# Kernel tuning notes

Measured on AMD Instinct MI355X. Metric: run time of the kernel, lower is better.

Reference implementation:

```python
import jax, jax.numpy as jnp
import numpy as np
from jax import lax

E, L, S, F = 4, 8, 512, 32
SAMPLE_SIZE = 512
BATCH_LEN = 64
TRAIN_ENVS = [0, 1, 2]


def setup_inputs() -> dict:
    key = jax.random.key(0)
    k1, k2 = jax.random.split(key)
    data_len = jax.random.randint(k2, (E, L), S // 2, S + 1).astype(jnp.int32)
    matrix = jax.random.normal(k1, (E, L, S, F), dtype=jnp.float32)
    # zero-pad samples beyond each (env,label) length, as shape_to_matrix does
    mask = (jnp.arange(S)[None, None, :, None] < data_len[:, :, None, None])
    matrix = matrix * mask.astype(jnp.float32)
    params = jnp.eye(F, dtype=jnp.float32)
    return {"matrix": matrix, "params": params, "data_len": data_len}


def _pair_indices():
    train_idx, test_idx = [], []
    for i in range(E):
        for j in range(E):
            idx = i * E + j
            if i < j:
                test_idx.append(idx)
                if i in TRAIN_ENVS and j in TRAIN_ENVS:
                    train_idx.append(idx)
    return np.array(train_idx), np.array(test_idx)


def reference(matrix, params, data_len):
    # normalize by mean per-(env,label,feature) std (torch.std is unbiased -> ddof=1)
    std = jnp.std(matrix, axis=2, ddof=1).mean()
    m = matrix / std
    bw = 1.06 * (S ** (-1.0 / 5.0)) * jnp.std(m, axis=2, ddof=1).mean()
    lenf = data_len.astype(jnp.float32)                     # [E,L]
    proj = jnp.einsum('elsf,fg->elsg', m, params)           # [E,L,S,F]

    left = lax.stop_gradient(proj.min())
    right = lax.stop_gradient(proj.max())
    delta = (right - left) / SAMPLE_SIZE
    grid = jnp.linspace(left, right, SAMPLE_SIZE)           # [G]
    divisor = jnp.sqrt(2.0 * jnp.pi) * bw

    n_chunks = SAMPLE_SIZE // BATCH_LEN
    grid_chunks = grid.reshape(n_chunks, BATCH_LEN)
    inv2bw2 = 0.5 / (bw * bw)
    pad_count = (float(S) - lenf)[:, :, None, None]         # [E,L,1,1]
    lend = lenf[:, :, None, None]

    def step(carry, pts):
        # Gaussian KDE kernel: offset^(d^2) == exp(-0.5*d^2/bw^2)
        d2 = (proj[..., None] - pts) ** 2                   # [E,L,S,F,C]
        ksum = jnp.exp(-inv2bw2 * d2).sum(axis=2)           # [E,L,F,C]
        corr = pad_count * jnp.exp(-inv2bw2 * pts ** 2)     # zero-padding correction
        red = (ksum - corr) / lend                          # [E,L,F,C]
        diff = jnp.abs(red[:, None] - red[None, :]).sum(-1) # [E,E,L,F]
        return carry + diff, None

    store, _ = lax.scan(step, jnp.zeros((E, E, L, F), dtype=proj.dtype), grid_chunks)
    store_dis = (store / divisor).reshape(E * E, L, F)

    train_idx, test_idx = _pair_indices()
    test_results = (store_dis[test_idx] * delta / 2.0).max(axis=0)    # [L,F]
    train_results = (store_dis[train_idx] * delta / 2.0).max(axis=0)  # [L,F]
    train_dis = train_results.max(axis=0).mean()
    test_dis = test_results.max(axis=0).mean()
    return train_results, test_results, train_dis, test_dis
```

## Files before the change

### kernel.cpp

```cpp
#include <hip/hip_runtime.h>
#include <float.h>


#if __has_builtin(__builtin_amdgcn_exp2f)
__device__ __forceinline__ float fast_exp2(float x) { return __builtin_amdgcn_exp2f(x); }
#else
__device__ __forceinline__ float fast_exp2(float x) { return exp2f(x); }
#endif

#define MAXR 150
#define PADL 160
#define HW   840
#define WOFF 163
#define WFULL 336

#define PT_OFF    0
#define SX_OFF    524288
#define SXX_OFF   532480
#define MIN_OFF   540672
#define MAX_OFF   540928
#define CNT_OFF   541184

__global__ __launch_bounds__(256) void stage_prep(const float* __restrict__ matrix,
                                                  const float* __restrict__ params,
                                                  float* __restrict__ PT,
                                                  float* __restrict__ sxg,
                                                  float* __restrict__ sxxg,
                                                  float* __restrict__ minp,
                                                  float* __restrict__ maxp,
                                                  int* __restrict__ counter) {
    __shared__ float M[64][33];
    __shared__ float Pm[32][32];
    __shared__ float sxr[8][32], sxxr[8][32];
    __shared__ float rmin[4], rmax[4];
    const int bid = blockIdx.x;
    const int s0 = (bid & 7) << 6;
    const int el = bid >> 3;
    const int t = threadIdx.x;
    if (bid == 0 && t == 0) *counter = 0;
    {
        const float4 v = reinterpret_cast<const float4*>(params)[t];
        const int base = t << 2;
        Pm[base >> 5][base & 31]       = v.x;
        Pm[base >> 5][(base & 31) + 1] = v.y;
        Pm[base >> 5][(base & 31) + 2] = v.z;
        Pm[base >> 5][(base & 31) + 3] = v.w;
    }
    const float4* mb4 = reinterpret_cast<const float4*>(matrix + (size_t)(el * 512 + s0) * 32);
    #pragma unroll
    for (int k = t; k < 512; k += 256) {
        const float4 v = mb4[k];
        const int base = k << 2;
        M[base >> 5][base & 31]       = v.x;
        M[base >> 5][(base & 31) + 1] = v.y;
        M[base >> 5][(base & 31) + 2] = v.z;
        M[base >> 5][(base & 31) + 3] = v.w;
    }
    __syncthreads();
    {
        const int f = t & 31, r = t >> 5;
        float sx = 0.f, sxx = 0.f;
        #pragma unroll
        for (int k = 0; k < 8; ++k) {
            float v = M[r * 8 + k][f];
            sx += v; sxx += v * v;
        }
        sxr[r][f] = sx; sxxr[r][f] = sxx;
    }
    const int s = t & 63;
    const int g0 = t >> 6;
    float lmin = FLT_MAX, lmax = -FLT_MAX;
    #pragma unroll
    for (int pass = 0; pass < 8; ++pass) {
        const int g = (pass << 2) + g0;
        float acc = 0.f;
        #pragma unroll
        for (int fp = 0; fp < 32; ++fp) acc += M[s][fp] * Pm[fp][g];
        lmin = fminf(lmin, acc);
        lmax = fmaxf(lmax, acc);
        PT[(size_t)(el * 32 + g) * 512 + s0 + s] = acc;
    }
    #pragma unroll
    for (int off = 32; off >= 1; off >>= 1) {
        lmin = fminf(lmin, __shfl_xor(lmin, off, 64));
        lmax = fmaxf(lmax, __shfl_xor(lmax, off, 64));
    }
    if ((t & 63) == 0) { rmin[t >> 6] = lmin; rmax[t >> 6] = lmax; }
    __syncthreads();
    if (t < 32) {
        float a = 0.f, b = 0.f;
        #pragma unroll
        for (int r = 0; r < 8; ++r) { a += sxr[r][t]; b += sxxr[r][t]; }
        sxg[bid * 32 + t] = a;
        sxxg[bid * 32 + t] = b;
    }
    if (t == 0) {
        minp[bid] = fminf(fminf(rmin[0], rmin[1]), fminf(rmin[2], rmin[3]));
        maxp[bid] = fmaxf(fmaxf(rmax[0], rmax[1]), fmaxf(rmax[2], rmax[3]));
    }
}

__global__ __launch_bounds__(512) void stage_kde3(const float* __restrict__ PT,
                                                  const float* __restrict__ sxg,
                                                  const float* __restrict__ sxxg,
                                                  const float* __restrict__ minp,
                                                  const float* __restrict__ maxp,
                                                  const int* __restrict__ dlen,
                                                  int* __restrict__ counter,
                                                  float* __restrict__ out) {
    __shared__ __align__(16) int   histI[4][HW];
    __shared__ __align__(16) float fine[4][512];
    __shared__ __align__(16) float wfull[WFULL];
    __shared__ float wsum[8], wmn[8], wmx[8];
    __shared__ float wred[8][6];
    __shared__ float csh[8];
    __shared__ int   Rsh;
    __shared__ int   lensh[4];
    __shared__ int   lastf;
    const int t = threadIdx.x;
    const int lf = blockIdx.x;
    const int l = lf >> 5, f = lf & 31;

    if (t < 4) lensh[t] = dlen[(t << 3) + l];
    {
        int* hflat = &histI[0][0];
        #pragma unroll
        for (int k = t; k < 4 * HW; k += 512) hflat[k] = 0;
    }

    {
        float sf = 0.f;
        #pragma unroll
        for (int tr = t; tr < 1024; tr += 512) {
            const int el = tr >> 5, fc = tr & 31;
            const int base = el * 256 + fc;
            float Sx = 0.f, Sxx = 0.f;
            #pragma unroll
            for (int tile = 0; tile < 8; ++tile) { Sx += sxg[base + tile * 32]; Sxx += sxxg[base + tile * 32]; }
            const float mean = Sx * (1.0f / 512.0f);
            const float var = (Sxx - Sx * mean) * (1.0f / 511.0f);
            sf += sqrtf(fmaxf(var, 0.f));
        }
        float mn = (t < 256) ? minp[t] : FLT_MAX;
        float mx = (t < 256) ? maxp[t] : -FLT_MAX;
        #pragma unroll
        for (int off = 32; off >= 1; off >>= 1) {
            sf += __shfl_xor(sf, off, 64);
            mn = fminf(mn, __shfl_xor(mn, off, 64));
            mx = fmaxf(mx, __shfl_xor(mx, off, 64));
        }
        if ((t & 63) == 0) { wsum[t >> 6] = sf; wmn[t >> 6] = mn; wmx[t >> 6] = mx; }
        __syncthreads();
        if (t == 0) {
            float s = 0.f, lo = FLT_MAX, hi = -FLT_MAX;
            #pragma unroll
            for (int w = 0; w < 8; ++w) {
                s += wsum[w]; lo = fminf(lo, wmn[w]); hi = fmaxf(hi, wmx[w]);
            }
            const float stdv = s * (1.0f / 1024.0f);
            const float left  = lo / stdv;
            const float right = hi / stdv;
            const float bw = 1.06f * 0.28717458874925877f;
            const float delta = (right - left) * (1.0f / 512.0f);
            const float gstep = (right - left) * (1.0f / 511.0f);
            const float divisor = 2.5066282746310002f * bw;
            const float cpos = (0.5f / (bw * bw)) * 1.4426950408889634f;
            const float kf = sqrtf(cpos);
            const float h = gstep * kf;
            csh[0] = left * kf;
            csh[1] = h;
            csh[2] = (1.0f / stdv) * kf;
            csh[3] = delta * 0.5f / divisor;
            csh[5] = 1.0f / h;
            Rsh = min((int)(3.5f / h) + 1, MAXR);
        }
    }
    __syncthreads();
    const float h = csh[1];
    const int R = Rsh;

    if (t < WFULL) {
        const int d = t - WOFF;
        const int ad = (d < 0) ? -d : d;
        const float u = (float)ad * h;
        wfull[t] = (ad <= R) ? fast_exp2(-(u * u)) : 0.f;
    }

    const int e = t >> 7;
    const int idx = t & 127;
    {
        const int sbase = idx << 2;
        const int lenE = lensh[e];
        const size_t row = ((size_t)(((e << 3) + l) * 32 + f) << 9);
        const float4 xv = *reinterpret_cast<const float4*>(&PT[row + sbase]);
        const float A = csh[2] * csh[5];
        const float B = csh[0] * csh[5];
        float uu[4] = { fmaf(xv.x, A, -B), fmaf(xv.y, A, -B),
                        fmaf(xv.z, A, -B), fmaf(xv.w, A, -B) };
        #pragma unroll
        for (int q = 0; q < 4; ++q) {
            if (sbase + q < lenE) {
                const float u = fminf(fmaxf(uu[q], 0.f), 511.f);
                const int   b = (int)u;
                const float fr = u - (float)b;
                const int w1 = (int)(fr * 16384.f + 0.5f);
                atomicAdd(&histI[e][PADL + b], 16384 - w1);
                atomicAdd(&histI[e][PADL + b + 1], w1);
            }
        }
    }
    __syncthreads();

    #pragma unroll
    for (int e2 = 0; e2 < 4; ++e2) {
        const float ce = (1.0f / 16384.0f) / (float)lensh[e2];
        for (int k = t; k < HW; k += 512) {
            const int iv = histI[e2][k];
            *reinterpret_cast<float*>(&histI[e2][k]) = (float)iv * ce;
        }
    }
    __syncthreads();

    {
        const float4* __restrict__ hf4 =
            reinterpret_cast<const float4*>(&histI[e][0]);
        const float4* __restrict__ wf4 = reinterpret_cast<const float4*>(&wfull[0]);
        const int hbase = 40 + idx;
        const int i_lo = -((R + 3) >> 2) - 1;
        const int i_hi = (R + 3) >> 2;
        float o0 = 0.f, o1 = 0.f, o2 = 0.f, o3 = 0.f;
        float4 W0 = wf4[40 + i_lo];
        for (int i = i_lo; i <= i_hi; ++i) {
            const float4 W1 = wf4[41 + i];
            const float4 H = hf4[hbase + i];
            o0 += H.x * W0.w + H.y * W1.x + H.z * W1.y + H.w * W1.z;
            o1 += H.x * W0.z + H.y * W0.w + H.z * W1.x + H.w * W1.y;
            o2 += H.x * W0.y + H.y * W0.z + H.z * W0.w + H.w * W1.x;
            o3 += H.x * W0.x + H.y * W0.y + H.z * W0.z + H.w * W0.w;
            W0 = W1;
        }
        *reinterpret_cast<float4*>(&fine[e][idx << 2]) = make_float4(o0, o1, o2, o3);
    }
    __syncthreads();

    {
        const float r0 = fine[0][t], r1 = fine[1][t], r2 = fine[2][t], r3 = fine[3][t];
        float pr[6];
        pr[0] = fabsf(r0 - r1);
        pr[1] = fabsf(r0 - r2);
        pr[2] = fabsf(r0 - r3);
        pr[3] = fabsf(r1 - r2);
        pr[4] = fabsf(r1 - r3);
        pr[5] = fabsf(r2 - r3);
        #pragma unroll
        for (int pi = 0; pi < 6; ++pi) {
            float v = pr[pi];
            #pragma unroll
            for (int off = 32; off >= 1; off >>= 1) v += __shfl_xor(v, off, 64);
            if ((t & 63) == 0) wred[t >> 6][pi] = v;
        }
    }
    __syncthreads();
    if (t == 0) {
        const float scale = csh[3];
        float v[6];
        #pragma unroll
        for (int pi = 0; pi < 6; ++pi) {
            float sm = 0.f;
            #pragma unroll
            for (int w = 0; w < 8; ++w) sm += wred[w][pi];
            v[pi] = sm * scale;
        }
        float testv = v[0];
        #pragma unroll
        for (int pi = 1; pi < 6; ++pi) testv = fmaxf(testv, v[pi]);
        const float trainv = fmaxf(fmaxf(v[0], v[1]), v[3]);
        out[lf] = trainv;
        out[256 + lf] = testv;
        __threadfence();
        const int old = __hip_atomic_fetch_add(counter, 1, __ATOMIC_ACQ_REL,
                                               __HIP_MEMORY_SCOPE_AGENT);
        lastf = (old == 255);
    }
    __syncthreads();

    if (lastf && t < 64) {
        const int ff = t & 31;
        const int base = (t >= 32) ? 256 : 0;
        float m = -FLT_MAX;
        #pragma unroll
        for (int ll = 0; ll < 8; ++ll) {
            const float val = __hip_atomic_load(&out[base + ll * 32 + ff],
                                                __ATOMIC_RELAXED, __HIP_MEMORY_SCOPE_AGENT);
            m = fmaxf(m, val);
        }
        #pragma unroll
        for (int off = 16; off >= 1; off >>= 1) m += __shfl_xor(m, off, 32);
        if (ff == 0) out[512 + (base ? 1 : 0)] = m * (1.0f / 32.0f);
    }
}

extern "C" void kernel_launch(void* const* d_in, const int* in_sizes, int n_in,
                              void* d_out, int out_size, void* d_ws, size_t ws_size,
                              hipStream_t stream) {
    (void)in_sizes; (void)n_in; (void)out_size; (void)ws_size;
    const float* matrix = (const float*)d_in[0];
    const float* params = (const float*)d_in[1];
    const int*   dlen   = (const int*)d_in[2];
    float* out = (float*)d_out;
    float* ws  = (float*)d_ws;
    float* PT   = ws + PT_OFF;
    float* sxg  = ws + SX_OFF;
    float* sxxg = ws + SXX_OFF;
    float* minp = ws + MIN_OFF;
    float* maxp = ws + MAX_OFF;
    int*   cnt  = (int*)(ws + CNT_OFF);

    hipLaunchKernelGGL(stage_prep, dim3(256), dim3(256), 0, stream,
                       matrix, params, PT, sxg, sxxg, minp, maxp, cnt);
    hipLaunchKernelGGL(stage_kde3, dim3(256), dim3(512), 0, stream,
                       PT, sxg, sxxg, minp, maxp, dlen, cnt, out);
}
```

Before: 82.42 us.

## Split KDE stage into constants, per-env histogram, and pairwise reduce kernels

Replaces the single 256-block KDE kernel with three kernels. A one-block kernel computes the global normalisation constants once instead of every block repeating the reduction. A 1024-block kernel builds one histogram and convolution per (env,label,feature), and a final 256-block kernel computes the pairwise absolute differences and the last reductions. This raises block-level parallelism and removes redundant constant computation, but adds two kernel launches and a global-memory round trip for the fine grids.

After: 84.47 us. 1.02x slower.

```diff
diff --git a/kernel.cpp b/kernel.cpp
--- a/kernel.cpp
+++ b/kernel.cpp
@@ -20,6 +20,8 @@
 #define MIN_OFF   540672
 #define MAX_OFF   540928
 #define CNT_OFF   541184
+#define CSH_OFF   541200
+#define FINE_OFF  541216
 
 __global__ __launch_bounds__(256) void stage_prep(const float* __restrict__ matrix,
                                                   const float* __restrict__ params,
@@ -100,132 +102,119 @@
     }
 }
 
-__global__ __launch_bounds__(512) void stage_kde3(const float* __restrict__ PT,
-                                                  const float* __restrict__ sxg,
-                                                  const float* __restrict__ sxxg,
-                                                  const float* __restrict__ minp,
-                                                  const float* __restrict__ maxp,
+__global__ __launch_bounds__(1024) void stage_consts(const float* __restrict__ sxg,
+                                                     const float* __restrict__ sxxg,
+                                                     const float* __restrict__ minp,
+                                                     const float* __restrict__ maxp,
+                                                     float* __restrict__ csh_g) {
+    __shared__ float wsum[16], wmn[16], wmx[16];
+    const int t = threadIdx.x;
+    float sf;
+    {
+        const int el = t >> 5, fc = t & 31;
+        const int base = el * 256 + fc;
+        float Sx = 0.f, Sxx = 0.f;
+        #pragma unroll
+        for (int tile = 0; tile < 8; ++tile) { Sx += sxg[base + tile * 32]; Sxx += sxxg[base + tile * 32]; }
+        const float mean = Sx * (1.0f / 512.0f);
+        const float var = (Sxx - Sx * mean) * (1.0f / 511.0f);
+        sf = sqrtf(fmaxf(var, 0.f));
+    }
+    float mn = (t < 256) ? minp[t] : FLT_MAX;
+    float mx = (t < 256) ? maxp[t] : -FLT_MAX;
+    #pragma unroll
+    for (int off = 32; off >= 1; off >>= 1) {
+        sf += __shfl_xor(sf, off, 64);
+        mn = fminf(mn, __shfl_xor(mn, off, 64));
+        mx = fmaxf(mx, __shfl_xor(mx, off, 64));
+    }
+    if ((t & 63) == 0) { wsum[t >> 6] = sf; wmn[t >> 6] = mn; wmx[t >> 6] = mx; }
+    __syncthreads();
+    if (t == 0) {
+        float s = 0.f, lo = FLT_MAX, hi = -FLT_MAX;
+        #pragma unroll
+        for (int w = 0; w < 16; ++w) {
+            s += wsum[w]; lo = fminf(lo, wmn[w]); hi = fmaxf(hi, wmx[w]);
+        }
+        const float stdv = s * (1.0f / 1024.0f);
+        const float left  = lo / stdv;
+        const float right = hi / stdv;
+        const float bw = 1.06f * 0.28717458874925877f;
+        const float delta = (right - left) * (1.0f / 512.0f);
+        const float gstep = (right - left) * (1.0f / 511.0f);
+        const float divisor = 2.5066282746310002f * bw;
+        const float cpos = (0.5f / (bw * bw)) * 1.4426950408889634f;
+        const float kf = sqrtf(cpos);
+        const float h = gstep * kf;
+        const float invh = 1.0f / h;
+        csh_g[0] = h;
+        csh_g[1] = (1.0f / stdv) * kf * invh;
+        csh_g[2] = left * kf * invh;
+        csh_g[3] = delta * 0.5f / divisor;
+        csh_g[4] = (float)min((int)(3.5f / h) + 1, MAXR);
+    }
+}
+
+__global__ __launch_bounds__(256) void stage_hist(const float* __restrict__ PT,
+                                                  const float* __restrict__ csh_g,
                                                   const int* __restrict__ dlen,
-                                                  int* __restrict__ counter,
-                                                  float* __restrict__ out) {
-    __shared__ __align__(16) int   histI[4][HW];
-    __shared__ __align__(16) float fine[4][512];
+                                                  float* __restrict__ fine_g) {
+    __shared__ __align__(16) int   histI[HW];
     __shared__ __align__(16) float wfull[WFULL];
-    __shared__ float wsum[8], wmn[8], wmx[8];
-    __shared__ float wred[8][6];
-    __shared__ float csh[8];
-    __shared__ int   Rsh;
-    __shared__ int   lensh[4];
-    __shared__ int   lastf;
     const int t = threadIdx.x;
-    const int lf = blockIdx.x;
+    const int bid = blockIdx.x;
+    const int e = bid & 3, lf = bid >> 2;
     const int l = lf >> 5, f = lf & 31;
 
-    if (t < 4) lensh[t] = dlen[(t << 3) + l];
-    {
-        int* hflat = &histI[0][0];
-        #pragma unroll
-        for (int k = t; k < 4 * HW; k += 512) hflat[k] = 0;
-    }
-
-    {
-        float sf = 0.f;
-        #pragma unroll
-        for (int tr = t; tr < 1024; tr += 512) {
-            const int el = tr >> 5, fc = tr & 31;
-            const int base = el * 256 + fc;
-            float Sx = 0.f, Sxx = 0.f;
-            #pragma unroll
-            for (int tile = 0; tile < 8; ++tile) { Sx += sxg[base + tile * 32]; Sxx += sxxg[base + tile * 32]; }
-            const float mean = Sx * (1.0f / 512.0f);
-            const float var = (Sxx - Sx * mean) * (1.0f / 511.0f);
-            sf += sqrtf(fmaxf(var, 0.f));
-        }
-        float mn = (t < 256) ? minp[t] : FLT_MAX;
-        float mx = (t < 256) ? maxp[t] : -FLT_MAX;
-        #pragma unroll
-        for (int off = 32; off >= 1; off >>= 1) {
-            sf += __shfl_xor(sf, off, 64);
-            mn = fminf(mn, __shfl_xor(mn, off, 64));
-            mx = fmaxf(mx, __shfl_xor(mx, off, 64));
-        }
-        if ((t & 63) == 0) { wsum[t >> 6] = sf; wmn[t >> 6] = mn; wmx[t >> 6] = mx; }
-        __syncthreads();
-        if (t == 0) {
-            float s = 0.f, lo = FLT_MAX, hi = -FLT_MAX;
-            #pragma unroll
-            for (int w = 0; w < 8; ++w) {
-                s += wsum[w]; lo = fminf(lo, wmn[w]); hi = fmaxf(hi, wmx[w]);
-            }
-            const float stdv = s * (1.0f / 1024.0f);
-            const float left  = lo / stdv;
-            const float right = hi / stdv;
-            const float bw = 1.06f * 0.28717458874925877f;
-            const float delta = (right - left) * (1.0f / 512.0f);
-            const float gstep = (right - left) * (1.0f / 511.0f);
-            const float divisor = 2.5066282746310002f * bw;
-            const float cpos = (0.5f / (bw * bw)) * 1.4426950408889634f;
-            const float kf = sqrtf(cpos);
-            const float h = gstep * kf;
-            csh[0] = left * kf;
-            csh[1] = h;
-            csh[2] = (1.0f / stdv) * kf;
-            csh[3] = delta * 0.5f / divisor;
-            csh[5] = 1.0f / h;
-            Rsh = min((int)(3.5f / h) + 1, MAXR);
-        }
-    }
-    __syncthreads();
-    const float h = csh[1];
-    const int R = Rsh;
-
-    if (t < WFULL) {
-        const int d = t - WOFF;
+    const float h = csh_g[0], A = csh_g[1], B = csh_g[2];
+    const int R = (int)csh_g[4];
+    const int lenE = dlen[(e << 3) + l];
+
+    #pragma unroll
+    for (int k = t; k < HW; k += 256) histI[k] = 0;
+    #pragma unroll
+    for (int k = t; k < WFULL; k += 256) {
+        const int d = k - WOFF;
         const int ad = (d < 0) ? -d : d;
         const float u = (float)ad * h;
-        wfull[t] = (ad <= R) ? fast_exp2(-(u * u)) : 0.f;
-    }
-
-    const int e = t >> 7;
-    const int idx = t & 127;
-    {
-        const int sbase = idx << 2;
-        const int lenE = lensh[e];
+        wfull[k] = (ad <= R) ? fast_exp2(-(u * u)) : 0.f;
+    }
+    __syncthreads();
+
+    {
         const size_t row = ((size_t)(((e << 3) + l) * 32 + f) << 9);
-        const float4 xv = *reinterpret_cast<const float4*>(&PT[row + sbase]);
-        const float A = csh[2] * csh[5];
-        const float B = csh[0] * csh[5];
-        float uu[4] = { fmaf(xv.x, A, -B), fmaf(xv.y, A, -B),
-                        fmaf(xv.z, A, -B), fmaf(xv.w, A, -B) };
-        #pragma unroll
-        for (int q = 0; q < 4; ++q) {
-            if (sbase + q < lenE) {
+        const float2 xv = *reinterpret_cast<const float2*>(&PT[row + (t << 1)]);
+        const float u0 = fmaf(xv.x, A, -B);
+        const float u1 = fmaf(xv.y, A, -B);
+        const float uu[2] = { u0, u1 };
+        #pragma unroll
+        for (int q = 0; q < 2; ++q) {
+            if ((t << 1) + q < lenE) {
                 const float u = fminf(fmaxf(uu[q], 0.f), 511.f);
                 const int   b = (int)u;
                 const float fr = u - (float)b;
                 const int w1 = (int)(fr * 16384.f + 0.5f);
-                atomicAdd(&histI[e][PADL + b], 16384 - w1);
-                atomicAdd(&histI[e][PADL + b + 1], w1);
+                atomicAdd(&histI[PADL + b], 16384 - w1);
+                atomicAdd(&histI[PADL + b + 1], w1);
             }
         }
     }
     __syncthreads();
 
-    #pragma unroll
-    for (int e2 = 0; e2 < 4; ++e2) {
-        const float ce = (1.0f / 16384.0f) / (float)lensh[e2];
-        for (int k = t; k < HW; k += 512) {
-            const int iv = histI[e2][k];
-            *reinterpret_cast<float*>(&histI[e2][k]) = (float)iv * ce;
-        }
-    }
-    __syncthreads();
-
-    {
-        const float4* __restrict__ hf4 =
-            reinterpret_cast<const float4*>(&histI[e][0]);
+    {
+        const float ce = (1.0f / 16384.0f) / (float)lenE;
+        #pragma unroll
+        for (int k = t; k < HW; k += 256) {
+            const int iv = histI[k];
+            *reinterpret_cast<float*>(&histI[k]) = (float)iv * ce;
+        }
+    }
+    __syncthreads();
+
+    if (t < 128) {
+        const float4* __restrict__ hf4 = reinterpret_cast<const float4*>(&histI[0]);
         const float4* __restrict__ wf4 = reinterpret_cast<const float4*>(&wfull[0]);
-        const int hbase = 40 + idx;
+        const int hbase = 40 + t;
         const int i_lo = -((R + 3) >> 2) - 1;
         const int i_hi = (R + 3) >> 2;
         float o0 = 0.f, o1 = 0.f, o2 = 0.f, o3 = 0.f;
@@ -239,30 +228,41 @@
             o3 += H.x * W0.x + H.y * W0.y + H.z * W0.z + H.w * W0.w;
             W0 = W1;
         }
-        *reinterpret_cast<float4*>(&fine[e][idx << 2]) = make_float4(o0, o1, o2, o3);
-    }
-    __syncthreads();
-
-    {
-        const float r0 = fine[0][t], r1 = fine[1][t], r2 = fine[2][t], r3 = fine[3][t];
-        float pr[6];
-        pr[0] = fabsf(r0 - r1);
-        pr[1] = fabsf(r0 - r2);
-        pr[2] = fabsf(r0 - r3);
-        pr[3] = fabsf(r1 - r2);
-        pr[4] = fabsf(r1 - r3);
-        pr[5] = fabsf(r2 - r3);
-        #pragma unroll
-        for (int pi = 0; pi < 6; ++pi) {
-            float v = pr[pi];
-            #pragma unroll
-            for (int off = 32; off >= 1; off >>= 1) v += __shfl_xor(v, off, 64);
-            if ((t & 63) == 0) wred[t >> 6][pi] = v;
-        }
+        *reinterpret_cast<float4*>(&fine_g[((size_t)bid << 9) + (t << 2)]) =
+            make_float4(o0, o1, o2, o3);
+    }
+}
+
+__global__ __launch_bounds__(512) void stage_reduce(const float* __restrict__ fine_g,
+                                                    const float* __restrict__ csh_g,
+                                                    int* __restrict__ counter,
+                                                    float* __restrict__ out) {
+    __shared__ float wred[8][6];
+    __shared__ int lastf;
+    const int t = threadIdx.x;
+    const int lf = blockIdx.x;
+    const size_t base4 = (size_t)(lf << 2) << 9;
+    const float r0 = fine_g[base4 + t];
+    const float r1 = fine_g[base4 + 512 + t];
+    const float r2 = fine_g[base4 + 1024 + t];
+    const float r3 = fine_g[base4 + 1536 + t];
+    float pr[6];
+    pr[0] = fabsf(r0 - r1);
+    pr[1] = fabsf(r0 - r2);
+    pr[2] = fabsf(r0 - r3);
+    pr[3] = fabsf(r1 - r2);
+    pr[4] = fabsf(r1 - r3);
+    pr[5] = fabsf(r2 - r3);
+    #pragma unroll
+    for (int pi = 0; pi < 6; ++pi) {
+        float v = pr[pi];
+        #pragma unroll
+        for (int off = 32; off >= 1; off >>= 1) v += __shfl_xor(v, off, 64);
+        if ((t & 63) == 0) wred[t >> 6][pi] = v;
     }
     __syncthreads();
     if (t == 0) {
-        const float scale = csh[3];
+        const float scale = csh_g[3];
         float v[6];
         #pragma unroll
         for (int pi = 0; pi < 6; ++pi) {
@@ -283,7 +283,6 @@
         lastf = (old == 255);
     }
     __syncthreads();
-
     if (lastf && t < 64) {
         const int ff = t & 31;
         const int base = (t >= 32) ? 256 : 0;
@@ -315,9 +314,15 @@
     float* minp = ws + MIN_OFF;
     float* maxp = ws + MAX_OFF;
     int*   cnt  = (int*)(ws + CNT_OFF);
-
-    hipLaunchKernelGGL(stage_prep, dim3(256), dim3(256), 0, stream,
+    float* cshg = ws + CSH_OFF;
+    float* fine = ws + FINE_OFF;
+
+    hipLaunchKernelGGL(stage_prep,   dim3(256),  dim3(256),  0, stream,
                        matrix, params, PT, sxg, sxxg, minp, maxp, cnt);
-    hipLaunchKernelGGL(stage_kde3, dim3(256), dim3(512), 0, stream,
-                       PT, sxg, sxxg, minp, maxp, dlen, cnt, out);
-}
+    hipLaunchKernelGGL(stage_consts, dim3(1),    dim3(1024), 0, stream,
+                       sxg, sxxg, minp, maxp, cshg);
+    hipLaunchKernelGGL(stage_hist,   dim3(1024), dim3(256),  0, stream,
+                       PT, cshg, dlen, fine);
+    hipLaunchKernelGGL(stage_reduce, dim3(256),  dim3(512),  0, stream,
+                       fine, cshg, cnt, out);
+}
```

## Convolve KDE at even grid points only and interpolate the odd points

Applied to the files above, without the earlier changes.

The KDE convolution stage now evaluates only every other grid point, using 256 threads. The odd grid points are filled in with a 4-tap cubic interpolation, with special weights at the boundaries. The histogram is accumulated with float LDS atomics pre-scaled by 1/len, which removes the integer-to-float conversion pass and one barrier. The prep kernel now does a register-blocked projection straight from global memory instead of staging the matrix in LDS. Interpolating the odd points adds approximation error on top of the existing binning approximation.

Result: slower. 84.20 us (+2.2%).

```diff
diff --git a/kernel.cpp b/kernel.cpp
--- a/kernel.cpp
+++ b/kernel.cpp
@@ -29,8 +29,7 @@
                                                   float* __restrict__ minp,
                                                   float* __restrict__ maxp,
                                                   int* __restrict__ counter) {
-    __shared__ float M[64][33];
-    __shared__ float Pm[32][32];
+    __shared__ float Pm[1024];
     __shared__ float sxr[8][32], sxxr[8][32];
     __shared__ float rmin[4], rmax[4];
     const int bid = blockIdx.x;
@@ -38,47 +37,50 @@
     const int el = bid >> 3;
     const int t = threadIdx.x;
     if (bid == 0 && t == 0) *counter = 0;
-    {
-        const float4 v = reinterpret_cast<const float4*>(params)[t];
-        const int base = t << 2;
-        Pm[base >> 5][base & 31]       = v.x;
-        Pm[base >> 5][(base & 31) + 1] = v.y;
-        Pm[base >> 5][(base & 31) + 2] = v.z;
-        Pm[base >> 5][(base & 31) + 3] = v.w;
-    }
-    const float4* mb4 = reinterpret_cast<const float4*>(matrix + (size_t)(el * 512 + s0) * 32);
-    #pragma unroll
-    for (int k = t; k < 512; k += 256) {
-        const float4 v = mb4[k];
-        const int base = k << 2;
-        M[base >> 5][base & 31]       = v.x;
-        M[base >> 5][(base & 31) + 1] = v.y;
-        M[base >> 5][(base & 31) + 2] = v.z;
-        M[base >> 5][(base & 31) + 3] = v.w;
-    }
-    __syncthreads();
+    reinterpret_cast<float4*>(Pm)[t] = reinterpret_cast<const float4*>(params)[t];
     {
         const int f = t & 31, r = t >> 5;
+        const float* mb = matrix + (size_t)(el * 512 + s0) * 32;
         float sx = 0.f, sxx = 0.f;
         #pragma unroll
         for (int k = 0; k < 8; ++k) {
-            float v = M[r * 8 + k][f];
+            const float v = mb[(r * 8 + k) * 32 + f];
             sx += v; sxx += v * v;
         }
         sxr[r][f] = sx; sxxr[r][f] = sxx;
     }
-    const int s = t & 63;
-    const int g0 = t >> 6;
+    __syncthreads();
+    const int gq = t >> 6, sl = t & 63;
+    const int s = s0 + sl;
+    float row[32];
+    {
+        const float4* rp = reinterpret_cast<const float4*>(matrix + ((size_t)(el * 512 + s) << 5));
+        #pragma unroll
+        for (int i = 0; i < 8; ++i) {
+            const float4 v = rp[i];
+            row[4 * i] = v.x; row[4 * i + 1] = v.y;
+            row[4 * i + 2] = v.z; row[4 * i + 3] = v.w;
+        }
+    }
+    float acc[8];
+    #pragma unroll
+    for (int j = 0; j < 8; ++j) acc[j] = 0.f;
+    const float4* pm4 = reinterpret_cast<const float4*>(Pm);
+    #pragma unroll
+    for (int fp = 0; fp < 32; ++fp) {
+        const float4 w0 = pm4[fp * 8 + gq * 2];
+        const float4 w1 = pm4[fp * 8 + gq * 2 + 1];
+        const float rv = row[fp];
+        acc[0] += rv * w0.x; acc[1] += rv * w0.y;
+        acc[2] += rv * w0.z; acc[3] += rv * w0.w;
+        acc[4] += rv * w1.x; acc[5] += rv * w1.y;
+        acc[6] += rv * w1.z; acc[7] += rv * w1.w;
+    }
     float lmin = FLT_MAX, lmax = -FLT_MAX;
     #pragma unroll
-    for (int pass = 0; pass < 8; ++pass) {
-        const int g = (pass << 2) + g0;
-        float acc = 0.f;
-        #pragma unroll
-        for (int fp = 0; fp < 32; ++fp) acc += M[s][fp] * Pm[fp][g];
-        lmin = fminf(lmin, acc);
-        lmax = fmaxf(lmax, acc);
-        PT[(size_t)(el * 32 + g) * 512 + s0 + s] = acc;
+    for (int j = 0; j < 8; ++j) {
+        PT[(size_t)(el * 32 + gq * 8 + j) * 512 + s] = acc[j];
+        lmin = fminf(lmin, acc[j]); lmax = fmaxf(lmax, acc[j]);
     }
     #pragma unroll
     for (int off = 32; off >= 1; off >>= 1) {
@@ -100,7 +102,7 @@
     }
 }
 
-__global__ __launch_bounds__(512) void stage_kde3(const float* __restrict__ PT,
+__global__ __launch_bounds__(512) void stage_kde4(const float* __restrict__ PT,
                                                   const float* __restrict__ sxg,
                                                   const float* __restrict__ sxxg,
                                                   const float* __restrict__ minp,
@@ -108,7 +110,7 @@
                                                   const int* __restrict__ dlen,
                                                   int* __restrict__ counter,
                                                   float* __restrict__ out) {
-    __shared__ __align__(16) int   histI[4][HW];
+    __shared__ __align__(16) float histF[4][HW];
     __shared__ __align__(16) float fine[4][512];
     __shared__ __align__(16) float wfull[WFULL];
     __shared__ float wsum[8], wmn[8], wmx[8];
@@ -123,9 +125,9 @@
 
     if (t < 4) lensh[t] = dlen[(t << 3) + l];
     {
-        int* hflat = &histI[0][0];
-        #pragma unroll
-        for (int k = t; k < 4 * HW; k += 512) hflat[k] = 0;
+        float4* hflat = reinterpret_cast<float4*>(&histF[0][0]);
+        #pragma unroll
+        for (int k = t; k < HW; k += 512) hflat[k] = make_float4(0.f, 0.f, 0.f, 0.f);
     }
 
     {
@@ -167,16 +169,16 @@
             const float cpos = (0.5f / (bw * bw)) * 1.4426950408889634f;
             const float kf = sqrtf(cpos);
             const float h = gstep * kf;
-            csh[0] = left * kf;
-            csh[1] = h;
-            csh[2] = (1.0f / stdv) * kf;
+            const float invh = 1.0f / h;
+            csh[0] = h;
+            csh[1] = (1.0f / stdv) * kf * invh;
+            csh[2] = left * kf * invh;
             csh[3] = delta * 0.5f / divisor;
-            csh[5] = 1.0f / h;
             Rsh = min((int)(3.5f / h) + 1, MAXR);
         }
     }
     __syncthreads();
-    const float h = csh[1];
+    const float h = csh[0], A = csh[1], B = csh[2];
     const int R = Rsh;
 
     if (t < WFULL) {
@@ -187,59 +189,67 @@
     }
 
     const int e = t >> 7;
-    const int idx = t & 127;
-    {
-        const int sbase = idx << 2;
+    {
+        const int sbase = (t & 127) << 2;
         const int lenE = lensh[e];
+        const float invLen = 1.0f / (float)lenE;
         const size_t row = ((size_t)(((e << 3) + l) * 32 + f) << 9);
         const float4 xv = *reinterpret_cast<const float4*>(&PT[row + sbase]);
-        const float A = csh[2] * csh[5];
-        const float B = csh[0] * csh[5];
-        float uu[4] = { fmaf(xv.x, A, -B), fmaf(xv.y, A, -B),
-                        fmaf(xv.z, A, -B), fmaf(xv.w, A, -B) };
+        const float uu[4] = { fmaf(xv.x, A, -B), fmaf(xv.y, A, -B),
+                              fmaf(xv.z, A, -B), fmaf(xv.w, A, -B) };
         #pragma unroll
         for (int q = 0; q < 4; ++q) {
             if (sbase + q < lenE) {
                 const float u = fminf(fmaxf(uu[q], 0.f), 511.f);
                 const int   b = (int)u;
                 const float fr = u - (float)b;
-                const int w1 = (int)(fr * 16384.f + 0.5f);
-                atomicAdd(&histI[e][PADL + b], 16384 - w1);
-                atomicAdd(&histI[e][PADL + b + 1], w1);
+                atomicAdd(&histF[e][PADL + b], (1.f - fr) * invLen);
+                atomicAdd(&histF[e][PADL + b + 1], fr * invLen);
             }
         }
     }
     __syncthreads();
 
-    #pragma unroll
-    for (int e2 = 0; e2 < 4; ++e2) {
-        const float ce = (1.0f / 16384.0f) / (float)lensh[e2];
-        for (int k = t; k < HW; k += 512) {
-            const int iv = histI[e2][k];
-            *reinterpret_cast<float*>(&histI[e2][k]) = (float)iv * ce;
-        }
-    }
-    __syncthreads();
-
-    {
-        const float4* __restrict__ hf4 =
-            reinterpret_cast<const float4*>(&histI[e][0]);
+    if (t < 256) {
+        const int e2 = t >> 6, tid = t & 63;
+        const float4* __restrict__ hf4 = reinterpret_cast<const float4*>(&histF[e2][0]);
         const float4* __restrict__ wf4 = reinterpret_cast<const float4*>(&wfull[0]);
-        const int hbase = 40 + idx;
-        const int i_lo = -((R + 3) >> 2) - 1;
-        const int i_hi = (R + 3) >> 2;
+        const int hb = 40 + 2 * tid;
+        const int i_lo = -((R + 6) >> 2);
+        const int i_hi = (R + 6) >> 2;
         float o0 = 0.f, o1 = 0.f, o2 = 0.f, o3 = 0.f;
-        float4 W0 = wf4[40 + i_lo];
+        float4 Wa = wf4[39 + i_lo];
+        float4 Wb = wf4[40 + i_lo];
         for (int i = i_lo; i <= i_hi; ++i) {
-            const float4 W1 = wf4[41 + i];
-            const float4 H = hf4[hbase + i];
-            o0 += H.x * W0.w + H.y * W1.x + H.z * W1.y + H.w * W1.z;
-            o1 += H.x * W0.z + H.y * W0.w + H.z * W1.x + H.w * W1.y;
-            o2 += H.x * W0.y + H.y * W0.z + H.z * W0.w + H.w * W1.x;
-            o3 += H.x * W0.x + H.y * W0.y + H.z * W0.z + H.w * W0.w;
-            W0 = W1;
-        }
-        *reinterpret_cast<float4*>(&fine[e][idx << 2]) = make_float4(o0, o1, o2, o3);
+            const float4 Wc = wf4[41 + i];
+            const float4 H = hf4[hb + i];
+            o0 += H.x * Wb.w + H.y * Wc.x + H.z * Wc.y + H.w * Wc.z;
+            o1 += H.x * Wb.y + H.y * Wb.z + H.z * Wb.w + H.w * Wc.x;
+            o2 += H.x * Wa.w + H.y * Wb.x + H.z * Wb.y + H.w * Wb.z;
+            o3 += H.x * Wa.y + H.y * Wa.z + H.z * Wa.w + H.w * Wb.x;
+            Wa = Wb; Wb = Wc;
+        }
+        const int gbase = (tid << 3);
+        fine[e2][gbase]     = o0;
+        fine[e2][gbase + 2] = o1;
+        fine[e2][gbase + 4] = o2;
+        fine[e2][gbase + 6] = o3;
+    }
+    __syncthreads();
+
+    #pragma unroll
+    for (int it = 0; it < 2; ++it) {
+        const int idx = t + 512 * it;
+        const int e3 = idx >> 8, k = idx & 255;
+        const int g = 2 * k + 1;
+        const int b = min(max(k - 1, 0), 252);
+        float4 W;
+        if (k == 0)        W = make_float4( 0.3125f,  0.9375f, -0.3125f,  0.0625f);
+        else if (k == 254) W = make_float4( 0.0625f, -0.3125f,  0.9375f,  0.3125f);
+        else if (k == 255) W = make_float4(-0.3125f,  1.3125f, -2.1875f,  2.1875f);
+        else               W = make_float4(-0.0625f,  0.5625f,  0.5625f, -0.0625f);
+        fine[e3][g] = W.x * fine[e3][2 * b]     + W.y * fine[e3][2 * b + 2]
+                    + W.z * fine[e3][2 * b + 4] + W.w * fine[e3][2 * b + 6];
     }
     __syncthreads();
 
@@ -283,7 +293,6 @@
         lastf = (old == 255);
     }
     __syncthreads();
-
     if (lastf && t < 64) {
         const int ff = t & 31;
         const int base = (t >= 32) ? 256 : 0;
@@ -318,6 +327,6 @@
 
     hipLaunchKernelGGL(stage_prep, dim3(256), dim3(256), 0, stream,
                        matrix, params, PT, sxg, sxxg, minp, maxp, cnt);
-    hipLaunchKernelGGL(stage_kde3, dim3(256), dim3(512), 0, stream,
+    hipLaunchKernelGGL(stage_kde4, dim3(256), dim3(512), 0, stream,
                        PT, sxg, sxxg, minp, maxp, dlen, cnt, out);
 }
```
